# Kernel optimization log

Measured on AMD Instinct MI355X. Metric: run time of the kernel, lower is better.

## Reference

```python
import jax, jax.numpy as jnp
import numpy as np
from jax import lax

T, A, F = 32, 32, 4          # tokens, analyses per token, feats per analysis
E = 256; FE = F * E          # feat emb dim, flattened analysis emb (1024)
H = 768; H2 = 2 * H          # encoder hidden (bi), decoder hidden 1536
DTOK = 256; DDEC = FE + DTOK # decoder input: analysis emb + token emb
V = 50000; VTOK = 30000


def setup_inputs() -> dict:
    key = jax.random.key(0)
    ks = jax.random.split(key, 16)
    g = lambda k, sh, s=0.02: (jax.random.normal(k, sh, jnp.float32) * s)
    return {
        "lattice": jax.random.randint(ks[0], (1, T, A, F), 0, V),
        "lattice_mask": jnp.ones((1, T, A), bool),
        "inputs": jax.random.randint(ks[1], (1, T), 0, VTOK),
        "input_lengths": jnp.full((1, 1, 1), T, jnp.int32),
        "gold_indices": jax.random.randint(ks[2], (1, T), 0, A),
        "sos_ids": jax.random.randint(ks[3], (F,), 0, V),
        "emb_table": g(ks[4], (V, E), 0.1),
        "tok_emb_table": g(ks[5], (VTOK, DTOK), 0.1),
        "enc_Wx_f": g(ks[6], (FE, 4 * H)),
        "enc_Wh_f": g(ks[7], (H, 4 * H)),
        "enc_b_f": jnp.zeros(4 * H, jnp.float32),
        "enc_Wx_b": g(ks[8], (FE, 4 * H)),
        "enc_Wh_b": g(ks[9], (H, 4 * H)),
        "enc_b_b": jnp.zeros(4 * H, jnp.float32),
        "dec_Wx": g(ks[10], (DDEC, 4 * H2)),
        "dec_Wh": g(ks[11], (H2, 4 * H2)),
        "dec_b": jnp.zeros(4 * H2, jnp.float32),
        "attn_W": g(ks[12], (H2, H2)),
    }


def _lstm(xs, Wx, Wh, b, hsize, reverse=False):
    # torch LSTM gate order: i, f, g, o
    def step(carry, x):
        h, c = carry
        gt = x @ Wx + h @ Wh + b
        i, f, g, o = jnp.split(gt, 4)
        c = jax.nn.sigmoid(f) * c + jax.nn.sigmoid(i) * jnp.tanh(g)
        h = jax.nn.sigmoid(o) * jnp.tanh(c)
        return (h, c), h
    init = (jnp.zeros(hsize, xs.dtype), jnp.zeros(hsize, xs.dtype))
    (h, c), ys = lax.scan(step, init, xs, reverse=reverse)
    return ys, h, c


def reference(lattice, lattice_mask, inputs, input_lengths, gold_indices, sos_ids,
              emb_table, tok_emb_table,
              enc_Wx_f, enc_Wh_f, enc_b_f, enc_Wx_b, enc_Wh_b, enc_b_b,
              dec_Wx, dec_Wh, dec_b, attn_W):
    # lattice_emb: per-feat embedding, flattened per analysis -> [1,T,A,FE]
    embed_lattice = emb_table[lattice].reshape(1, T, A, FE)
    # mask is all-True, so mask-packing == flatten: [T*A, FE]
    packed = embed_lattice.reshape(T * A, FE)
    ys_f, hf, cf = _lstm(packed, enc_Wx_f, enc_Wh_f, enc_b_f, H)
    ys_b, hb, cb = _lstm(packed, enc_Wx_b, enc_Wh_b, enc_b_b, H, reverse=True)
    enc = jnp.concatenate([ys_f, ys_b], axis=-1).reshape(T, A, H2)  # per-token slices
    h0 = jnp.concatenate([hf, hb])  # decoder init = concat(fwd,bwd) final states
    c0 = jnp.concatenate([cf, cb])
    tok_emb = tok_emb_table[inputs[0]]          # [T, DTOK]
    sos_emb = emb_table[sos_ids].reshape(FE)    # SOS analysis embedding
    lat = embed_lattice[0]                      # [T, A, FE]

    def step(carry, xs_t):
        h, c, prev = carry
        enc_t, tok_t, g_t, lat_t = xs_t
        x = jnp.concatenate([prev, tok_t])      # [DDEC]
        gt = x @ dec_Wx + h @ dec_Wh + dec_b
        i, f, g, o = jnp.split(gt, 4)
        c_n = jax.nn.sigmoid(f) * c + jax.nn.sigmoid(i) * jnp.tanh(g)
        h_n = jax.nn.sigmoid(o) * jnp.tanh(c_n)
        score = (h_n @ attn_W) @ enc_t.T        # bilinear attention scores [A]
        # teacher forcing: next analysis emb gathered by gold index
        return (h_n, c_n, lat_t[g_t]), score

    _, scores = lax.scan(step, (h0, c0, sos_emb), (enc, tok_emb, gold_indices[0], lat))
    return scores[None]  # [1, T, A]
```

## Files before the change

kernel.cpp:

```cpp
#include <hip/hip_runtime.h>
#include <cstddef>
#include <cstdint>

#define T_ 32
#define A_ 32
#define F_ 4
#define E_ 256
#define FE_ 1024
#define H_ 768
#define H2_ 1536
#define G4_ 3072
#define G8_ 6144
#define DTOK_ 256
#define DDEC_ 1280
#define SEQ_ 1024

constexpr size_t OFF_PACKED  = 0;
constexpr size_t OFF_XF      = OFF_PACKED + 1024ull*1024;
constexpr size_t OFF_XB      = OFF_XF + 1024ull*3072;
constexpr size_t OFF_XD      = OFF_XB + 1024ull*3072;
constexpr size_t OFF_XDIN    = OFF_XD + 32*6144;
constexpr size_t OFF_ENC     = OFF_XDIN + 32*1280;
constexpr size_t OFF_HN      = OFF_ENC + 1024ull*1536;
constexpr size_t OFF_AMAT    = OFF_HN + 32*1536;
constexpr size_t OFF_C0      = OFF_AMAT + 32*1536;
constexpr size_t OFF_PAIRS_E = OFF_C0 + 1536;
constexpr size_t OFF_PAIRS_D = OFF_PAIRS_E + 6144;
constexpr size_t MEMSET_BYTES = (6144 + 6144) * 4;

__device__ __forceinline__ float sigf(float x) { return 1.f / (1.f + __expf(-x)); }

__global__ void embed_k(const int* __restrict__ lattice, const int* __restrict__ inputs,
                        const int* __restrict__ gold, const int* __restrict__ sos,
                        const float* __restrict__ emb, const float* __restrict__ tok_emb,
                        float* __restrict__ packed, float* __restrict__ xdec_in) {
    int b = blockIdx.x, tid = threadIdx.x;
    if (b < SEQ_) {
        #pragma unroll
        for (int f = 0; f < F_; ++f) {
            int vid = lattice[b * F_ + f];
            packed[(size_t)b * FE_ + f * E_ + tid] = emb[(size_t)vid * E_ + tid];
        }
    } else {
        int t = b - SEQ_;
        for (int j = tid; j < DDEC_; j += 256) {
            float v;
            if (j < FE_) {
                int f = j >> 8, e2 = j & 255;
                int vid = (t == 0) ? sos[f]
                                   : lattice[(((t - 1) * A_) + gold[t - 1]) * F_ + f];
                v = emb[(size_t)vid * E_ + e2];
            } else {
                v = tok_emb[(size_t)inputs[t] * DTOK_ + (j - FE_)];
            }
            xdec_in[(size_t)t * DDEC_ + j] = v;
        }
    }
}

#define BM 128
#define BN 128
#define BK 8
__device__ __forceinline__ void gemm_body(
    const float* __restrict__ A, const float* __restrict__ B,
    const float* __restrict__ bias, float* __restrict__ C,
    int M, int N, int K, int n0, int m0) {
    __shared__ float As[BK][BM + 4];
    __shared__ float Bs[BK][BN + 4];
    int tid = threadIdx.x;
    int tx = tid & 15, ty = tid >> 4;
    int lam = tid >> 1, lak = (tid & 1) * 4;
    int lbk = tid >> 5, lbn = (tid & 31) * 4;
    float acc[8][8] = {};
    for (int k0 = 0; k0 < K; k0 += BK) {
        float4 av = make_float4(0.f, 0.f, 0.f, 0.f);
        if (m0 + lam < M)
            av = *(const float4*)(A + (size_t)(m0 + lam) * K + k0 + lak);
        float4 bv = *(const float4*)(B + (size_t)(k0 + lbk) * N + n0 + lbn);
        __syncthreads();
        As[lak + 0][lam] = av.x; As[lak + 1][lam] = av.y;
        As[lak + 2][lam] = av.z; As[lak + 3][lam] = av.w;
        *(float4*)&Bs[lbk][lbn] = bv;
        __syncthreads();
        #pragma unroll
        for (int kk = 0; kk < BK; ++kk) {
            float a[8], b[8];
            *(float4*)&a[0] = *(const float4*)&As[kk][ty * 8];
            *(float4*)&a[4] = *(const float4*)&As[kk][ty * 8 + 4];
            *(float4*)&b[0] = *(const float4*)&Bs[kk][tx * 8];
            *(float4*)&b[4] = *(const float4*)&Bs[kk][tx * 8 + 4];
            #pragma unroll
            for (int i = 0; i < 8; ++i)
                #pragma unroll
                for (int j = 0; j < 8; ++j)
                    acc[i][j] += a[i] * b[j];
        }
    }
    #pragma unroll
    for (int i = 0; i < 8; ++i) {
        int m = m0 + ty * 8 + i;
        if (m >= M) break;
        #pragma unroll
        for (int j = 0; j < 8; ++j) {
            int n = n0 + tx * 8 + j;
            float bb = bias ? bias[n] : 0.f;
            C[(size_t)m * N + n] = acc[i][j] + bb;
        }
    }
}

__global__ __launch_bounds__(256) void gemm_bias_k(
    const float* __restrict__ A, const float* __restrict__ B,
    const float* __restrict__ bias, float* __restrict__ C, int M, int N, int K) {
    gemm_body(A, B, bias, C, M, N, K, blockIdx.x * BN, blockIdx.y * BM);
}

__global__ __launch_bounds__(256) void gemm_bias2_k(
    const float* __restrict__ A,
    const float* __restrict__ B0, const float* __restrict__ bias0, float* __restrict__ C0,
    const float* __restrict__ B1, const float* __restrict__ bias1, float* __restrict__ C1,
    int M, int N, int K) {
    const float* B = blockIdx.z ? B1 : B0;
    const float* bias = blockIdx.z ? bias1 : bias0;
    float* C = blockIdx.z ? C1 : C0;
    gemm_body(A, B, bias, C, M, N, K, blockIdx.x * BN, blockIdx.y * BM);
}

__global__ __launch_bounds__(768, 1) void lstm_enc_k(
    const float* __restrict__ Xf, const float* __restrict__ Xb,
    const float* __restrict__ Whf, const float* __restrict__ Whb,
    float* __restrict__ enc, unsigned long long* __restrict__ pairsE,
    unsigned long long* __restrict__ pairsD, float* __restrict__ c0) {
    const int dir = blockIdx.x >> 6;
    const int wb  = blockIdx.x & 63;
    const float* X  = dir ? Xb : Xf;
    const float* Wh = dir ? Whb : Whf;
    unsigned long long* pp = pairsE + (size_t)dir * (2 * 768);
    const int tid = threadIdx.x;
    const int out = tid >> 4, kl = tid & 15;
    const int q = out / 12, jj = out - q * 12;
    const int col = q * H_ + wb * 12 + jj;
    const int xcol = (tid / 12) * H_ + wb * 12 + (tid % 12);

    float w[12][4];
    #pragma unroll
    for (int i = 0; i < 12; ++i) {
        int kb = kl * 4 + 64 * i;
        #pragma unroll
        for (int e = 0; e < 4; ++e)
            w[i][e] = Wh[(size_t)(kb + e) * G4_ + col];
    }

    __shared__ float h_s[768];
    __shared__ float gbuf[48];
    __shared__ float xs[48];
    float c = 0.f;

    for (int t = 0; t < SEQ_; ++t) {
        const int row = dir ? (SEQ_ - 1 - t) : t;
        float xv = 0.f;
        if (tid < 48) xv = X[(size_t)row * G4_ + xcol];

        unsigned long long* p = pp + (size_t)(t & 1) * 768 + tid;
        unsigned long long v = __hip_atomic_load(p, __ATOMIC_RELAXED, __HIP_MEMORY_SCOPE_AGENT);
        while ((unsigned)(v >> 32) != (unsigned)t)
            v = __hip_atomic_load(p, __ATOMIC_RELAXED, __HIP_MEMORY_SCOPE_AGENT);
        h_s[tid] = __uint_as_float((unsigned)v);
        __syncthreads();

        float s = 0.f;
        #pragma unroll
        for (int i = 0; i < 12; ++i) {
            const float4 hv = *(const float4*)&h_s[kl * 4 + 64 * i];
            s += w[i][0] * hv.x + w[i][1] * hv.y + w[i][2] * hv.z + w[i][3] * hv.w;
        }
        s += __shfl_xor(s, 1); s += __shfl_xor(s, 2);
        s += __shfl_xor(s, 4); s += __shfl_xor(s, 8);
        if (kl == 0) gbuf[out] = s;
        if (tid < 48) xs[tid] = xv;
        __syncthreads();

        if (tid < 12) {
            float iv = gbuf[tid]      + xs[tid];
            float fv = gbuf[12 + tid] + xs[12 + tid];
            float gv = gbuf[24 + tid] + xs[24 + tid];
            float ov = gbuf[36 + tid] + xs[36 + tid];
            c = sigf(fv) * c + sigf(iv) * tanhf(gv);
            float h = sigf(ov) * tanhf(c);
            int jg = wb * 12 + tid;
            enc[(size_t)row * H2_ + dir * H_ + jg] = h;
            unsigned long long pk =
                ((unsigned long long)(unsigned)(t + 1) << 32) | (unsigned long long)__float_as_uint(h);
            __hip_atomic_store(pp + (size_t)((t + 1) & 1) * 768 + jg, pk,
                               __ATOMIC_RELAXED, __HIP_MEMORY_SCOPE_AGENT);
            if (t == SEQ_ - 1) {
                __hip_atomic_store(pairsD + (size_t)(dir * H_ + jg),
                                   (unsigned long long)__float_as_uint(h),
                                   __ATOMIC_RELAXED, __HIP_MEMORY_SCOPE_AGENT);
                c0[dir * H_ + jg] = c;
            }
        }
    }
}

__global__ __launch_bounds__(768, 1) void lstm_dec_k(
    const float* __restrict__ Xd, const float* __restrict__ Wh,
    float* __restrict__ Hn, unsigned long long* __restrict__ pairs,
    const float* __restrict__ c0) {
    const int wb = blockIdx.x;
    const int tid = threadIdx.x;
    const int out = tid >> 4, kl = tid & 15;
    const int q = out / 12, jj = out - q * 12;
    const int col = q * H2_ + wb * 12 + jj;
    const int xcol = (tid / 12) * H2_ + wb * 12 + (tid % 12);

    float w[24][4];
    #pragma unroll
    for (int i = 0; i < 24; ++i) {
        int kb = kl * 4 + 64 * i;
        #pragma unroll
        for (int e = 0; e < 4; ++e)
            w[i][e] = Wh[(size_t)(kb + e) * G8_ + col];
    }

    __shared__ float h_s[1536];
    __shared__ float gbuf[48];
    __shared__ float xs[48];
    float c = (tid < 12) ? c0[wb * 12 + tid] : 0.f;

    for (int t = 0; t < T_; ++t) {
        float xv = 0.f;
        if (tid < 48) xv = Xd[(size_t)t * G8_ + xcol];

        unsigned long long* p0 = pairs + (size_t)(t & 1) * 1536 + tid;
        unsigned long long v0 = __hip_atomic_load(p0, __ATOMIC_RELAXED, __HIP_MEMORY_SCOPE_AGENT);
        while ((unsigned)(v0 >> 32) != (unsigned)t)
            v0 = __hip_atomic_load(p0, __ATOMIC_RELAXED, __HIP_MEMORY_SCOPE_AGENT);
        unsigned long long* p1 = p0 + 768;
        unsigned long long v1 = __hip_atomic_load(p1, __ATOMIC_RELAXED, __HIP_MEMORY_SCOPE_AGENT);
        while ((unsigned)(v1 >> 32) != (unsigned)t)
            v1 = __hip_atomic_load(p1, __ATOMIC_RELAXED, __HIP_MEMORY_SCOPE_AGENT);
        h_s[tid]       = __uint_as_float((unsigned)v0);
        h_s[tid + 768] = __uint_as_float((unsigned)v1);
        __syncthreads();

        float s = 0.f;
        #pragma unroll
        for (int i = 0; i < 24; ++i) {
            const float4 hv = *(const float4*)&h_s[kl * 4 + 64 * i];
            s += w[i][0] * hv.x + w[i][1] * hv.y + w[i][2] * hv.z + w[i][3] * hv.w;
        }
        s += __shfl_xor(s, 1); s += __shfl_xor(s, 2);
        s += __shfl_xor(s, 4); s += __shfl_xor(s, 8);
        if (kl == 0) gbuf[out] = s;
        if (tid < 48) xs[tid] = xv;
        __syncthreads();

        if (tid < 12) {
            float iv = gbuf[tid]      + xs[tid];
            float fv = gbuf[12 + tid] + xs[12 + tid];
            float gv = gbuf[24 + tid] + xs[24 + tid];
            float ov = gbuf[36 + tid] + xs[36 + tid];
            c = sigf(fv) * c + sigf(iv) * tanhf(gv);
            float h = sigf(ov) * tanhf(c);
            int jg = wb * 12 + tid;
            Hn[(size_t)t * H2_ + jg] = h;
            unsigned long long pk =
                ((unsigned long long)(unsigned)(t + 1) << 32) | (unsigned long long)__float_as_uint(h);
            __hip_atomic_store(pairs + (size_t)((t + 1) & 1) * 1536 + jg, pk,
                               __ATOMIC_RELAXED, __HIP_MEMORY_SCOPE_AGENT);
        }
    }
}

__global__ void score_k(const float* __restrict__ Amat, const float* __restrict__ enc,
                        float* __restrict__ outp) {
    int t = blockIdx.x, tid = threadIdx.x;
    __shared__ float a_s[H2_];
    for (int i = tid; i < H2_; i += 256) a_s[i] = Amat[(size_t)t * H2_ + i];
    __syncthreads();
    int aa = tid >> 3, p = tid & 7;
    const float4* e = (const float4*)(enc + (size_t)(t * A_ + aa) * H2_ + p * 192);
    const float4* ap = (const float4*)(a_s + p * 192);
    float s = 0.f;
    #pragma unroll
    for (int i = 0; i < 48; ++i) {
        float4 av = ap[i], ev = e[i];
        s += av.x * ev.x + av.y * ev.y + av.z * ev.z + av.w * ev.w;
    }
    s += __shfl_xor(s, 1); s += __shfl_xor(s, 2); s += __shfl_xor(s, 4);
    if (p == 0) outp[t * A_ + aa] = s;
}

extern "C" void kernel_launch(void* const* d_in, const int* in_sizes, int n_in,
                              void* d_out, int out_size, void* d_ws, size_t ws_size,
                              hipStream_t stream) {
    const int*   lattice = (const int*)d_in[0];
    const int*   inputs  = (const int*)d_in[2];
    const int*   gold    = (const int*)d_in[4];
    const int*   sos     = (const int*)d_in[5];
    const float* emb     = (const float*)d_in[6];
    const float* tok     = (const float*)d_in[7];
    const float* Wxf = (const float*)d_in[8];
    const float* Whf = (const float*)d_in[9];
    const float* bf  = (const float*)d_in[10];
    const float* Wxb = (const float*)d_in[11];
    const float* Whb = (const float*)d_in[12];
    const float* bb  = (const float*)d_in[13];
    const float* dWx = (const float*)d_in[14];
    const float* dWh = (const float*)d_in[15];
    const float* db  = (const float*)d_in[16];
    const float* aW  = (const float*)d_in[17];
    float* ws  = (float*)d_ws;
    float* out = (float*)d_out;

    float* packed = ws + OFF_PACKED;
    float* Xf     = ws + OFF_XF;
    float* Xb     = ws + OFF_XB;
    float* Xd     = ws + OFF_XD;
    float* xdin   = ws + OFF_XDIN;
    float* enc    = ws + OFF_ENC;
    float* Hn     = ws + OFF_HN;
    float* Amat   = ws + OFF_AMAT;
    float* c0     = ws + OFF_C0;
    unsigned long long* pairsE = (unsigned long long*)(ws + OFF_PAIRS_E);
    unsigned long long* pairsD = (unsigned long long*)(ws + OFF_PAIRS_D);

    hipMemsetAsync((char*)d_ws + OFF_PAIRS_E * sizeof(float), 0, MEMSET_BYTES, stream);

    embed_k<<<SEQ_ + T_, 256, 0, stream>>>(lattice, inputs, gold, sos, emb, tok,
                                           packed, xdin);
    gemm_bias2_k<<<dim3(G4_ / BN, SEQ_ / BM, 2), 256, 0, stream>>>(
        packed, Wxf, bf, Xf, Wxb, bb, Xb, SEQ_, G4_, FE_);
    gemm_bias_k<<<dim3(G8_ / BN, 1), 256, 0, stream>>>(xdin, dWx, db, Xd,
                                                       T_, G8_, DDEC_);
    lstm_enc_k<<<128, 768, 0, stream>>>(Xf, Xb, Whf, Whb, enc, pairsE, pairsD, c0);
    lstm_dec_k<<<128, 768, 0, stream>>>(Xd, dWh, Hn, pairsD, c0);
    gemm_bias_k<<<dim3(H2_ / BN, 1), 256, 0, stream>>>(Hn, aW, nullptr, Amat,
                                                       T_, H2_, H2_);
    score_k<<<T_, 256, 0, stream>>>(Amat, enc, out);
}
```

Before: 2.894 ms.

## Restructure LSTM recurrence to one wavefront per hidden unit with permuted gate layout

The input-projection GEMM epilogue now writes gate pre-activations in a permuted layout so the four gates of each hidden unit sit next to each other. The encoder and decoder recurrent kernels are rewritten so each 64-lane wavefront owns one hidden unit and computes all four gate dot-products itself. A full-wave shuffle reduction replaces the shared-memory gate buffer and the second __syncthreads per step, and shared h is double-buffered by step parity. The intent is to shorten the serial per-step critical path, at the cost of a longer shuffle reduction and strided scattered stores in the GEMM epilogue.

Result: slower. 5.056 ms (+74.7%).

```diff
diff --git a/kernel.cpp b/kernel.cpp
--- a/kernel.cpp
+++ b/kernel.cpp
@@ -64,7 +64,7 @@
 __device__ __forceinline__ void gemm_body(
     const float* __restrict__ A, const float* __restrict__ B,
     const float* __restrict__ bias, float* __restrict__ C,
-    int M, int N, int K, int n0, int m0) {
+    int M, int N, int K, int n0, int m0, int swh) {
     __shared__ float As[BK][BM + 4];
     __shared__ float Bs[BK][BN + 4];
     int tid = threadIdx.x;
@@ -96,6 +96,8 @@
                     acc[i][j] += a[i] * b[j];
         }
     }
+    int qg = 0, jb = 0;
+    if (swh) { qg = n0 / swh; jb = n0 - qg * swh; }
     #pragma unroll
     for (int i = 0; i < 8; ++i) {
         int m = m0 + ty * 8 + i;
@@ -104,26 +106,32 @@
         for (int j = 0; j < 8; ++j) {
             int n = n0 + tx * 8 + j;
             float bb = bias ? bias[n] : 0.f;
-            C[(size_t)m * N + n] = acc[i][j] + bb;
+            float v = acc[i][j] + bb;
+            if (swh) {
+                int jc = jb + tx * 8 + j;
+                n = (jc / 12) * 48 + (jc % 12) * 4 + qg;
+            }
+            C[(size_t)m * N + n] = v;
         }
     }
 }
 
 __global__ __launch_bounds__(256) void gemm_bias_k(
     const float* __restrict__ A, const float* __restrict__ B,
-    const float* __restrict__ bias, float* __restrict__ C, int M, int N, int K) {
-    gemm_body(A, B, bias, C, M, N, K, blockIdx.x * BN, blockIdx.y * BM);
+    const float* __restrict__ bias, float* __restrict__ C,
+    int M, int N, int K, int swh) {
+    gemm_body(A, B, bias, C, M, N, K, blockIdx.x * BN, blockIdx.y * BM, swh);
 }
 
 __global__ __launch_bounds__(256) void gemm_bias2_k(
     const float* __restrict__ A,
     const float* __restrict__ B0, const float* __restrict__ bias0, float* __restrict__ C0,
     const float* __restrict__ B1, const float* __restrict__ bias1, float* __restrict__ C1,
-    int M, int N, int K) {
+    int M, int N, int K, int swh) {
     const float* B = blockIdx.z ? B1 : B0;
     const float* bias = blockIdx.z ? bias1 : bias0;
     float* C = blockIdx.z ? C1 : C0;
-    gemm_body(A, B, bias, C, M, N, K, blockIdx.x * BN, blockIdx.y * BM);
+    gemm_body(A, B, bias, C, M, N, K, blockIdx.x * BN, blockIdx.y * BM, swh);
 }
 
 __global__ __launch_bounds__(768, 1) void lstm_enc_k(
@@ -135,63 +143,63 @@
     const int wb  = blockIdx.x & 63;
     const float* X  = dir ? Xb : Xf;
     const float* Wh = dir ? Whb : Whf;
-    unsigned long long* pp = pairsE + (size_t)dir * (2 * 768);
+    unsigned long long* pp = pairsE + (size_t)dir * 1536;
     const int tid = threadIdx.x;
-    const int out = tid >> 4, kl = tid & 15;
-    const int q = out / 12, jj = out - q * 12;
-    const int col = q * H_ + wb * 12 + jj;
-    const int xcol = (tid / 12) * H_ + wb * 12 + (tid % 12);
-
-    float w[12][4];
+    const int w = tid >> 6, lane = tid & 63, q4 = lane & 3;
+    const int jg = wb * 12 + w;
+
+    float wgt[3][4][4];
     #pragma unroll
-    for (int i = 0; i < 12; ++i) {
-        int kb = kl * 4 + 64 * i;
-        #pragma unroll
-        for (int e = 0; e < 4; ++e)
-            w[i][e] = Wh[(size_t)(kb + e) * G4_ + col];
-    }
-
-    __shared__ float h_s[768];
-    __shared__ float gbuf[48];
-    __shared__ float xs[48];
+    for (int i = 0; i < 3; ++i)
+        #pragma unroll
+        for (int e = 0; e < 4; ++e) {
+            int k = 4 * lane + e + 256 * i;
+            #pragma unroll
+            for (int g = 0; g < 4; ++g)
+                wgt[i][e][g] = Wh[(size_t)k * G4_ + g * H_ + jg];
+        }
+
+    __shared__ float h_s[2][768];
     float c = 0.f;
 
     for (int t = 0; t < SEQ_; ++t) {
         const int row = dir ? (SEQ_ - 1 - t) : t;
-        float xv = 0.f;
-        if (tid < 48) xv = X[(size_t)row * G4_ + xcol];
-
-        unsigned long long* p = pp + (size_t)(t & 1) * 768 + tid;
+        float xq = X[(size_t)row * G4_ + wb * 48 + w * 4 + q4];
+
+        const int par = t & 1;
+        unsigned long long* p = pp + par * 768 + tid;
         unsigned long long v = __hip_atomic_load(p, __ATOMIC_RELAXED, __HIP_MEMORY_SCOPE_AGENT);
         while ((unsigned)(v >> 32) != (unsigned)t)
             v = __hip_atomic_load(p, __ATOMIC_RELAXED, __HIP_MEMORY_SCOPE_AGENT);
-        h_s[tid] = __uint_as_float((unsigned)v);
+        h_s[par][tid] = __uint_as_float((unsigned)v);
         __syncthreads();
 
-        float s = 0.f;
-        #pragma unroll
-        for (int i = 0; i < 12; ++i) {
-            const float4 hv = *(const float4*)&h_s[kl * 4 + 64 * i];
-            s += w[i][0] * hv.x + w[i][1] * hv.y + w[i][2] * hv.z + w[i][3] * hv.w;
-        }
-        s += __shfl_xor(s, 1); s += __shfl_xor(s, 2);
-        s += __shfl_xor(s, 4); s += __shfl_xor(s, 8);
-        if (kl == 0) gbuf[out] = s;
-        if (tid < 48) xs[tid] = xv;
-        __syncthreads();
-
-        if (tid < 12) {
-            float iv = gbuf[tid]      + xs[tid];
-            float fv = gbuf[12 + tid] + xs[12 + tid];
-            float gv = gbuf[24 + tid] + xs[24 + tid];
-            float ov = gbuf[36 + tid] + xs[36 + tid];
-            c = sigf(fv) * c + sigf(iv) * tanhf(gv);
-            float h = sigf(ov) * tanhf(c);
-            int jg = wb * 12 + tid;
+        float a0 = 0.f, a1 = 0.f, a2 = 0.f, a3 = 0.f;
+        #pragma unroll
+        for (int i = 0; i < 3; ++i) {
+            const float4 hv = *(const float4*)&h_s[par][4 * lane + 256 * i];
+            a0 += wgt[i][0][0] * hv.x + wgt[i][1][0] * hv.y + wgt[i][2][0] * hv.z + wgt[i][3][0] * hv.w;
+            a1 += wgt[i][0][1] * hv.x + wgt[i][1][1] * hv.y + wgt[i][2][1] * hv.z + wgt[i][3][1] * hv.w;
+            a2 += wgt[i][0][2] * hv.x + wgt[i][1][2] * hv.y + wgt[i][2][2] * hv.z + wgt[i][3][2] * hv.w;
+            a3 += wgt[i][0][3] * hv.x + wgt[i][1][3] * hv.y + wgt[i][2][3] * hv.z + wgt[i][3][3] * hv.w;
+        }
+        #pragma unroll
+        for (int m = 1; m < 64; m <<= 1) {
+            a0 += __shfl_xor(a0, m); a1 += __shfl_xor(a1, m);
+            a2 += __shfl_xor(a2, m); a3 += __shfl_xor(a3, m);
+        }
+        float sg = (q4 == 0) ? a0 : (q4 == 1) ? a1 : (q4 == 2) ? a2 : a3;
+        sg += xq;
+        float tr = (q4 == 2) ? tanhf(sg) : sigf(sg);
+        float I  = __shfl(tr, 0), Fv = __shfl(tr, 1);
+        float G  = __shfl(tr, 2), O  = __shfl(tr, 3);
+        c = Fv * c + I * G;
+        float h = O * tanhf(c);
+        if (lane == 0) {
             enc[(size_t)row * H2_ + dir * H_ + jg] = h;
             unsigned long long pk =
                 ((unsigned long long)(unsigned)(t + 1) << 32) | (unsigned long long)__float_as_uint(h);
-            __hip_atomic_store(pp + (size_t)((t + 1) & 1) * 768 + jg, pk,
+            __hip_atomic_store(pp + ((t + 1) & 1) * 768 + jg, pk,
                                __ATOMIC_RELAXED, __HIP_MEMORY_SCOPE_AGENT);
             if (t == SEQ_ - 1) {
                 __hip_atomic_store(pairsD + (size_t)(dir * H_ + jg),
@@ -209,65 +217,65 @@
     const float* __restrict__ c0) {
     const int wb = blockIdx.x;
     const int tid = threadIdx.x;
-    const int out = tid >> 4, kl = tid & 15;
-    const int q = out / 12, jj = out - q * 12;
-    const int col = q * H2_ + wb * 12 + jj;
-    const int xcol = (tid / 12) * H2_ + wb * 12 + (tid % 12);
-
-    float w[24][4];
+    const int w = tid >> 6, lane = tid & 63, q4 = lane & 3;
+    const int jg = wb * 12 + w;
+
+    float wgt[6][4][4];
     #pragma unroll
-    for (int i = 0; i < 24; ++i) {
-        int kb = kl * 4 + 64 * i;
-        #pragma unroll
-        for (int e = 0; e < 4; ++e)
-            w[i][e] = Wh[(size_t)(kb + e) * G8_ + col];
-    }
-
-    __shared__ float h_s[1536];
-    __shared__ float gbuf[48];
-    __shared__ float xs[48];
-    float c = (tid < 12) ? c0[wb * 12 + tid] : 0.f;
+    for (int i = 0; i < 6; ++i)
+        #pragma unroll
+        for (int e = 0; e < 4; ++e) {
+            int k = 4 * lane + e + 256 * i;
+            #pragma unroll
+            for (int g = 0; g < 4; ++g)
+                wgt[i][e][g] = Wh[(size_t)k * G8_ + g * H2_ + jg];
+        }
+
+    __shared__ float h_s[2][1536];
+    float c = c0[jg];
 
     for (int t = 0; t < T_; ++t) {
-        float xv = 0.f;
-        if (tid < 48) xv = Xd[(size_t)t * G8_ + xcol];
-
-        unsigned long long* p0 = pairs + (size_t)(t & 1) * 1536 + tid;
+        float xq = Xd[(size_t)t * G8_ + wb * 48 + w * 4 + q4];
+
+        const int par = t & 1;
+        unsigned long long* p0 = pairs + par * 1536 + tid;
+        unsigned long long* p1 = p0 + 768;
         unsigned long long v0 = __hip_atomic_load(p0, __ATOMIC_RELAXED, __HIP_MEMORY_SCOPE_AGENT);
+        unsigned long long v1 = __hip_atomic_load(p1, __ATOMIC_RELAXED, __HIP_MEMORY_SCOPE_AGENT);
         while ((unsigned)(v0 >> 32) != (unsigned)t)
             v0 = __hip_atomic_load(p0, __ATOMIC_RELAXED, __HIP_MEMORY_SCOPE_AGENT);
-        unsigned long long* p1 = p0 + 768;
-        unsigned long long v1 = __hip_atomic_load(p1, __ATOMIC_RELAXED, __HIP_MEMORY_SCOPE_AGENT);
         while ((unsigned)(v1 >> 32) != (unsigned)t)
             v1 = __hip_atomic_load(p1, __ATOMIC_RELAXED, __HIP_MEMORY_SCOPE_AGENT);
-        h_s[tid]       = __uint_as_float((unsigned)v0);
-        h_s[tid + 768] = __uint_as_float((unsigned)v1);
+        h_s[par][tid]       = __uint_as_float((unsigned)v0);
+        h_s[par][tid + 768] = __uint_as_float((unsigned)v1);
         __syncthreads();
 
-        float s = 0.f;
-        #pragma unroll
-        for (int i = 0; i < 24; ++i) {
-            const float4 hv = *(const float4*)&h_s[kl * 4 + 64 * i];
-            s += w[i][0] * hv.x + w[i][1] * hv.y + w[i][2] * hv.z + w[i][3] * hv.w;
-        }
-        s += __shfl_xor(s, 1); s += __shfl_xor(s, 2);
-        s += __shfl_xor(s, 4); s += __shfl_xor(s, 8);
-        if (kl == 0) gbuf[out] = s;
-        if (tid < 48) xs[tid] = xv;
-        __syncthreads();
-
-        if (tid < 12) {
-            float iv = gbuf[tid]      + xs[tid];
-            float fv = gbuf[12 + tid] + xs[12 + tid];
-            float gv = gbuf[24 + tid] + xs[24 + tid];
-            float ov = gbuf[36 + tid] + xs[36 + tid];
-            c = sigf(fv) * c + sigf(iv) * tanhf(gv);
-            float h = sigf(ov) * tanhf(c);
-            int jg = wb * 12 + tid;
+        float a0 = 0.f, a1 = 0.f, a2 = 0.f, a3 = 0.f;
+        #pragma unroll
+        for (int i = 0; i < 6; ++i) {
+            const float4 hv = *(const float4*)&h_s[par][4 * lane + 256 * i];
+            a0 += wgt[i][0][0] * hv.x + wgt[i][1][0] * hv.y + wgt[i][2][0] * hv.z + wgt[i][3][0] * hv.w;
+            a1 += wgt[i][0][1] * hv.x + wgt[i][1][1] * hv.y + wgt[i][2][1] * hv.z + wgt[i][3][1] * hv.w;
+            a2 += wgt[i][0][2] * hv.x + wgt[i][1][2] * hv.y + wgt[i][2][2] * hv.z + wgt[i][3][2] * hv.w;
+            a3 += wgt[i][0][3] * hv.x + wgt[i][1][3] * hv.y + wgt[i][2][3] * hv.z + wgt[i][3][3] * hv.w;
+        }
+        #pragma unroll
+        for (int m = 1; m < 64; m <<= 1) {
+            a0 += __shfl_xor(a0, m); a1 += __shfl_xor(a1, m);
+            a2 += __shfl_xor(a2, m); a3 += __shfl_xor(a3, m);
+        }
+        float sg = (q4 == 0) ? a0 : (q4 == 1) ? a1 : (q4 == 2) ? a2 : a3;
+        sg += xq;
+        float tr = (q4 == 2) ? tanhf(sg) : sigf(sg);
+        float I  = __shfl(tr, 0), Fv = __shfl(tr, 1);
+        float G  = __shfl(tr, 2), O  = __shfl(tr, 3);
+        c = Fv * c + I * G;
+        float h = O * tanhf(c);
+        if (lane == 0) {
             Hn[(size_t)t * H2_ + jg] = h;
             unsigned long long pk =
                 ((unsigned long long)(unsigned)(t + 1) << 32) | (unsigned long long)__float_as_uint(h);
-            __hip_atomic_store(pairs + (size_t)((t + 1) & 1) * 1536 + jg, pk,
+            __hip_atomic_store(pairs + ((t + 1) & 1) * 1536 + jg, pk,
                                __ATOMIC_RELAXED, __HIP_MEMORY_SCOPE_AGENT);
         }
     }
@@ -331,12 +339,12 @@
     embed_k<<<SEQ_ + T_, 256, 0, stream>>>(lattice, inputs, gold, sos, emb, tok,
                                            packed, xdin);
     gemm_bias2_k<<<dim3(G4_ / BN, SEQ_ / BM, 2), 256, 0, stream>>>(
-        packed, Wxf, bf, Xf, Wxb, bb, Xb, SEQ_, G4_, FE_);
+        packed, Wxf, bf, Xf, Wxb, bb, Xb, SEQ_, G4_, FE_, H_);
     gemm_bias_k<<<dim3(G8_ / BN, 1), 256, 0, stream>>>(xdin, dWx, db, Xd,
-                                                       T_, G8_, DDEC_);
+                                                       T_, G8_, DDEC_, H2_);
     lstm_enc_k<<<128, 768, 0, stream>>>(Xf, Xb, Whf, Whb, enc, pairsE, pairsD, c0);
     lstm_dec_k<<<128, 768, 0, stream>>>(Xd, dWh, Hn, pairsD, c0);
     gemm_bias_k<<<dim3(H2_ / BN, 1), 256, 0, stream>>>(Hn, aW, nullptr, Amat,
-                                                       T_, H2_, H2_);
+                                                       T_, H2_, H2_, 0);
     score_k<<<T_, 256, 0, stream>>>(Amat, enc, out);
 }
```
